# Kernel tuning notes

Measured on AMD Instinct MI355X. Metric: run time of the kernel, lower is better.

Reference implementation:

```python
import jax, jax.numpy as jnp
import numpy as np

E, NH, NL, NP = 256, 8, 4, 4
D = E // NH
SPATIAL_SHAPES = np.array([[100, 134], [50, 67], [25, 34], [13, 17]], dtype=np.int64)
B = 2


def setup_inputs() -> dict:
    key = jax.random.key(0)
    ks = jax.random.split(key, 12)
    Lin = int((SPATIAL_SHAPES[:, 0] * SPATIAL_SHAPES[:, 1]).sum())
    Lq = Lin
    s = 0.02
    return {
        'query': jax.random.normal(ks[0], (Lq, B, E), jnp.float32),
        'value': jax.random.normal(ks[1], (Lin, B, E), jnp.float32),
        'reference_points': jax.random.uniform(ks[2], (B, Lq, NL, 2), jnp.float32),
        'spatial_shapes': SPATIAL_SHAPES,
        'W_value': jax.random.normal(ks[3], (E, E), jnp.float32) * s,
        'b_value': jnp.zeros((E,), jnp.float32),
        'W_offset': jax.random.normal(ks[4], (E, NH * NL * NP * 2), jnp.float32) * s,
        'b_offset': jax.random.normal(ks[5], (NH * NL * NP * 2,), jnp.float32) * 0.5,
        'W_attn': jax.random.normal(ks[6], (E, NH * NL * NP), jnp.float32) * s,
        'b_attn': jnp.zeros((NH * NL * NP,), jnp.float32),
        'W_out': jax.random.normal(ks[7], (E, E), jnp.float32) * s,
        'b_out': jnp.zeros((E,), jnp.float32),
    }


def _ms_deform_attn(value, spatial_shapes, sampling_locations, attention_weights):
    # value: (B, Lin, NH, D); sampling_locations: (B, Lq, NH, NL, NP, 2) in [0,1]
    # attention_weights: (B, Lq, NH, NL, NP)
    b, _, nh, d = value.shape
    lq = sampling_locations.shape[1]
    npnt = sampling_locations.shape[4]
    shapes = np.asarray(spatial_shapes)
    out = jnp.zeros((b, nh, lq, d), value.dtype)
    start = 0
    for l in range(shapes.shape[0]):
        H, W = int(shapes[l, 0]), int(shapes[l, 1])
        vl = value[:, start:start + H * W].transpose(0, 2, 1, 3)  # (B, NH, H*W, D)
        loc = sampling_locations[:, :, :, l].transpose(0, 2, 1, 3, 4)  # (B, NH, Lq, P, 2)
        # grid_sample align_corners=False convention (matches CUDA kernel)
        x = loc[..., 0] * W - 0.5
        y = loc[..., 1] * H - 0.5
        x0 = jnp.floor(x)
        y0 = jnp.floor(y)
        dx = x - x0
        dy = y - y0
        x0i = x0.astype(jnp.int32)
        y0i = y0.astype(jnp.int32)
        acc = jnp.zeros((b, nh, lq, npnt, d), value.dtype)
        corners = [
            (x0i, y0i, (1.0 - dx) * (1.0 - dy)),
            (x0i + 1, y0i, dx * (1.0 - dy)),
            (x0i, y0i + 1, (1.0 - dx) * dy),
            (x0i + 1, y0i + 1, dx * dy),
        ]
        for xi, yi, w in corners:
            valid = ((xi >= 0) & (xi < W) & (yi >= 0) & (yi < H)).astype(value.dtype)
            idx = jnp.clip(yi, 0, W - 1 if False else H - 1) * 0  # placeholder removed below
            idx = jnp.clip(yi, 0, H - 1) * W + jnp.clip(xi, 0, W - 1)  # (B, NH, Lq, P)
            g = jnp.take_along_axis(vl, idx.reshape(b, nh, -1)[..., None], axis=2)
            g = g.reshape(b, nh, lq, npnt, d)
            acc = acc + g * (w * valid)[..., None]
        awl = attention_weights[:, :, :, l].transpose(0, 2, 1, 3)  # (B, NH, Lq, P)
        out = out + jnp.einsum('bhqpd,bhqp->bhqd', acc, awl)
        start += H * W
    return out.transpose(0, 2, 1, 3).reshape(b, lq, nh * d)  # (B, Lq, E)


def reference(query, value, reference_points, spatial_shapes,
              W_value, b_value, W_offset, b_offset, W_attn, b_attn, W_out, b_out):
    q = query.transpose(1, 0, 2)   # (B, Lq, E)
    v = value.transpose(1, 0, 2)   # (B, Lin, E)
    b, lq, _ = q.shape
    lin = v.shape[1]
    v = (v @ W_value + b_value).reshape(b, lin, NH, D)
    offsets = (q @ W_offset + b_offset).reshape(b, lq, NH, NL, NP, 2)
    attn = (q @ W_attn + b_attn).reshape(b, lq, NH, NL, NP)
    attn = jax.nn.softmax(attn, axis=-1)  # softmax over points (as in source)
    shapes_f = jnp.asarray(np.asarray(spatial_shapes), jnp.float32)
    offset_normalizer = jnp.stack([shapes_f[:, 1], shapes_f[:, 0]], -1)  # (NL, 2) = (w, h)
    loc = reference_points[:, :, None, :, None, :] + offsets / offset_normalizer[None, None, None, :, None, :]
    out = _ms_deform_attn(v, spatial_shapes, loc, attn)  # (B, Lq, E)
    out = out @ W_out + b_out
    return out.transpose(1, 0, 2)  # (Lq, B, E)
```

## Files before the change

### kernel.cpp

```cpp
#include <hip/hip_runtime.h>
#include <math.h>

#define LQ    17821
#define MROWS 35642
#define KD    256

typedef __attribute__((ext_vector_type(8))) short bf16x8;
typedef __attribute__((ext_vector_type(4))) float f32x4;

__device__ __forceinline__ short f2bf(float f) {
  union { float f; unsigned u; } c; c.f = f;
  unsigned u = c.u;
  return (short)((u + 0x7fffu + ((u >> 16) & 1u)) >> 16);
}
__device__ __forceinline__ float bf2f(short s) {
  union { unsigned u; float f; } c;
  c.u = ((unsigned)(unsigned short)s) << 16;
  return c.f;
}

__global__ __launch_bounds__(256) void wtrans_all(
    const float* __restrict__ Wv, const float* __restrict__ Woff,
    const float* __restrict__ Wat, const float* __restrict__ Wout,
    const float* __restrict__ boff, const float* __restrict__ bat,
    short* __restrict__ wT, float* __restrict__ fbias)
{
  int sel = blockIdx.y;
  int idx = blockIdx.x * 256 + threadIdx.x;
  if (sel == 4) {
    if (idx < 384) fbias[idx] = (idx < 256) ? boff[idx] : bat[idx - 256];
    return;
  }
  const float* W = sel == 0 ? Wv : sel == 1 ? Woff : sel == 2 ? Wat : Wout;
  short* Wt = wT + (sel == 0 ? 0 : sel == 1 ? 65536 : sel == 2 ? 131072 : 163840);
  int N = (sel == 2) ? 128 : 256;
  if (idx < N * 256) {
    int n = idx >> 8, k = idx & 255;
    Wt[idx] = f2bf(W[k * N + n]);
  }
}

template<bool A_F32>
__global__ __launch_bounds__(256, 2) void gemm_fullk(
    const void* __restrict__ A0, const void* __restrict__ A1,
    const short* __restrict__ Bt0, const short* __restrict__ Bt1,
    const float* __restrict__ bias0, const float* __restrict__ bias1,
    short* __restrict__ out0, float* __restrict__ out1,
    int M, int N1, int gybase)
{
  __shared__ bf16x8 As[32 * 128];

  const int tid = threadIdx.x;
  const int gy = blockIdx.y + gybase;
  const bool sel0 = gy < 2;
  const void* A = sel0 ? A0 : A1;
  const short* Bt = sel0 ? Bt0 : Bt1;
  const float* bias = sel0 ? bias0 : bias1;
  const int bn = (sel0 ? gy : gy - 2) * 128;
  const int bm = blockIdx.x * 128;

  {
    const int r = tid >> 1;
    const int h2 = tid & 1;
    const size_t arow = (size_t)min(bm + r, M - 1) * KD;
#pragma unroll
    for (int i = 0; i < 16; ++i) {
      const int s = h2 * 16 + i;
      bf16x8 v;
      if (A_F32) {
        const float* ap = (const float*)A + arow + s * 8;
        float4 p0 = *(const float4*)ap;
        float4 p1 = *(const float4*)(ap + 4);
        v[0] = f2bf(p0.x); v[1] = f2bf(p0.y); v[2] = f2bf(p0.z); v[3] = f2bf(p0.w);
        v[4] = f2bf(p1.x); v[5] = f2bf(p1.y); v[6] = f2bf(p1.z); v[7] = f2bf(p1.w);
      } else {
        v = *(const bf16x8*)((const short*)A + arow + s * 8);
      }
      As[s * 128 + (r ^ (s & 7))] = v;
    }
  }
  __syncthreads();

  const int lane = tid & 63;
  const int wave = tid >> 6;
  const int wm = (wave & 1) * 64;
  const int wn = (wave >> 1) * 64;
  const int ln = lane & 15;
  const int lq = lane >> 4;

  f32x4 acc[4][4];
#pragma unroll
  for (int i = 0; i < 4; ++i)
#pragma unroll
    for (int j = 0; j < 4; ++j) acc[i][j] = (f32x4){0.f, 0.f, 0.f, 0.f};

  bf16x8 af[2][4], bf[2][4];

#define LD_A(kk, dst)                                                        \
  {                                                                          \
    const int sA = (kk) * 4 + lq;                                            \
    const int swz = sA & 7;                                                  \
    _Pragma("unroll")                                                        \
    for (int i = 0; i < 4; ++i)                                              \
      dst[i] = As[sA * 128 + ((wm + i * 16 + ln) ^ swz)];                    \
  }
#define LD_B(kk, dst)                                                        \
  {                                                                          \
    _Pragma("unroll")                                                        \
    for (int j = 0; j < 4; ++j)                                              \
      dst[j] = *(const bf16x8*)(Bt + (size_t)(bn + wn + j * 16 + ln) * KD +  \
                                (kk) * 32 + lq * 8);                         \
  }

  LD_A(0, af[0]);
  LD_B(0, bf[0]);
#pragma unroll
  for (int kk = 0; kk < 8; ++kk) {
    const int cur = kk & 1, nxt = cur ^ 1;
    if (kk < 7) {
      LD_B(kk + 1, bf[nxt]);
      LD_A(kk + 1, af[nxt]);
    }
#pragma unroll
    for (int i = 0; i < 4; ++i)
#pragma unroll
      for (int j = 0; j < 4; ++j)
        acc[i][j] = __builtin_amdgcn_mfma_f32_16x16x32_bf16(af[cur][i], bf[cur][j], acc[i][j], 0, 0, 0);
  }
#undef LD_A
#undef LD_B

  const int N = sel0 ? 256 : N1;
#pragma unroll
  for (int j = 0; j < 4; ++j) {
    const int col = bn + wn + j * 16 + ln;
    const float bb = bias[col];
#pragma unroll
    for (int i = 0; i < 4; ++i) {
      const int row0 = bm + wm + i * 16 + lq * 4;
#pragma unroll
      for (int r = 0; r < 4; ++r) {
        const int row = row0 + r;
        if (row < M) {
          float v = acc[i][j][r] + bb;
          if (sel0)
            out0[(size_t)row * 256 + col] = f2bf(v);
          else
            out1[(size_t)row * N + col] = v;
        }
      }
    }
  }
}

__global__ __launch_bounds__(256) void msda_sample(
    const short* __restrict__ vproj, const float* __restrict__ oa,
    const float* __restrict__ refp, short* __restrict__ out)
{
  static constexpr int LVL_H[4] = {100, 50, 25, 13};
  static constexpr int LVL_W[4] = {134, 67, 34, 17};
  static constexpr int LVL_S[4] = {0, 13400, 16750, 17600};

  __shared__ int4   s_off[8 * 8 * 17];
  __shared__ float4 s_w[8 * 8 * 17];

  const int tid = threadIdx.x;
  const int m0 = blockIdx.x * 8;

#pragma unroll
  for (int it = 0; it < 4; ++it) {
    int w = tid + it * 256;
    int mr = w >> 7;
    int rest = w & 127;
    int h = rest >> 4;
    int lp = rest & 15;
    int l = lp >> 2;
    int p = lp & 3;
    int m = m0 + mr;
    if (m < MROWS) {
      int b = m & 1, q = m >> 1;
      const int Hl = LVL_H[l], Wl = LVL_W[l], Sl = LVL_S[l];
      const float fW = (float)Wl, fH = (float)Hl;

      float4 av = *(const float4*)(oa + (size_t)m * 384 + 256 + h * 16 + l * 4);
      float a0 = av.x, a1 = av.y, a2 = av.z, a3 = av.w;
      float mx = fmaxf(fmaxf(a0, a1), fmaxf(a2, a3));
      a0 = __expf(a0 - mx); a1 = __expf(a1 - mx);
      a2 = __expf(a2 - mx); a3 = __expf(a3 - mx);
      float sel = (p == 0) ? a0 : (p == 1) ? a1 : (p == 2) ? a2 : a3;
      float aw = sel / (a0 + a1 + a2 + a3);

      const float* oPtr = oa + (size_t)m * 384 + h * 32 + l * 8 + p * 2;
      float ox = oPtr[0], oy = oPtr[1];
      const float* rPtr = refp + ((size_t)b * LQ + q) * 8 + l * 2;
      float rx = rPtr[0], ry = rPtr[1];

      float x = (rx + ox / fW) * fW - 0.5f;
      float y = (ry + oy / fH) * fH - 0.5f;
      float x0f = floorf(x), y0f = floorf(y);
      float dx = x - x0f, dy = y - y0f;
      int x0 = (int)x0f, y0 = (int)y0f;
      int x1 = x0 + 1, y1 = y0 + 1;

      float w00 = (1.f - dx) * (1.f - dy) * aw;
      float w10 = dx * (1.f - dy) * aw;
      float w01 = (1.f - dx) * dy * aw;
      float w11 = dx * dy * aw;

      bool vx0 = (x0 >= 0) & (x0 < Wl);
      bool vx1 = (x1 >= 0) & (x1 < Wl);
      bool vy0 = (y0 >= 0) & (y0 < Hl);
      bool vy1 = (y1 >= 0) & (y1 < Hl);
      int cx0 = min(max(x0, 0), Wl - 1);
      int cx1 = min(max(x1, 0), Wl - 1);
      int cy0 = min(max(y0, 0), Hl - 1);
      int cy1 = min(max(y1, 0), Hl - 1);

      int r0 = Sl + cy0 * Wl;
      int r1 = Sl + cy1 * Wl;
      int e = (mr * 8 + h) * 17 + lp;
      s_off[e] = make_int4(((r0 + cx0) * 2 + b) << 8,
                           ((r0 + cx1) * 2 + b) << 8,
                           ((r1 + cx0) * 2 + b) << 8,
                           ((r1 + cx1) * 2 + b) << 8);
      s_w[e] = make_float4((vy0 & vx0) ? w00 : 0.f,
                           (vy0 & vx1) ? w10 : 0.f,
                           (vy1 & vx0) ? w01 : 0.f,
                           (vy1 & vx1) ? w11 : 0.f);
    }
  }
  __syncthreads();

  const int mr = tid >> 5;
  const int t = tid & 31;
  const int h = t >> 2;
  const int dq = t & 3;
  const int m = m0 + mr;
  if (m >= MROWS) return;

  const int laneOff = h * 32 + dq * 8;
  const int ebase = (mr * 8 + h) * 17;
  float acc[8];
#pragma unroll
  for (int e = 0; e < 8; ++e) acc[e] = 0.f;

#pragma unroll 4
  for (int lp = 0; lp < 16; ++lp) {
    int4 off = s_off[ebase + lp];
    float4 wv = s_w[ebase + lp];
    bf16x8 u00 = *(const bf16x8*)(vproj + off.x + laneOff);
    bf16x8 u10 = *(const bf16x8*)(vproj + off.y + laneOff);
    bf16x8 u01 = *(const bf16x8*)(vproj + off.z + laneOff);
    bf16x8 u11 = *(const bf16x8*)(vproj + off.w + laneOff);
#pragma unroll
    for (int e = 0; e < 8; ++e) {
      acc[e] = fmaf(wv.x, bf2f(u00[e]), acc[e]);
      acc[e] = fmaf(wv.y, bf2f(u10[e]), acc[e]);
      acc[e] = fmaf(wv.z, bf2f(u01[e]), acc[e]);
      acc[e] = fmaf(wv.w, bf2f(u11[e]), acc[e]);
    }
  }

  bf16x8 o;
#pragma unroll
  for (int e = 0; e < 8; ++e) o[e] = f2bf(acc[e]);
  *(bf16x8*)(out + (size_t)m * 256 + laneOff) = o;
}

extern "C" void kernel_launch(void* const* d_in, const int* in_sizes, int n_in,
                              void* d_out, int out_size, void* d_ws, size_t ws_size,
                              hipStream_t stream)
{
  const float* query = (const float*)d_in[0];
  const float* value = (const float*)d_in[1];
  const float* refp  = (const float*)d_in[2];
  const float* Wv   = (const float*)d_in[4];
  const float* bv   = (const float*)d_in[5];
  const float* Woff = (const float*)d_in[6];
  const float* boff = (const float*)d_in[7];
  const float* Wat  = (const float*)d_in[8];
  const float* bat  = (const float*)d_in[9];
  const float* Wout = (const float*)d_in[10];
  const float* bout = (const float*)d_in[11];
  float* out = (float*)d_out;

  const size_t NELT = (size_t)MROWS * 256;
  short* wT    = (short*)d_ws;
  float* fbias = (float*)(wT + 229376);
  short* vproj = (short*)(fbias + 384);
  short* accb  = vproj + NELT;
  float* oa    = (float*)(accb + NELT);

  dim3 blk(256, 1, 1);
  int gm = (MROWS + 127) / 128;

  wtrans_all<<<dim3(256, 5), blk, 0, stream>>>(Wv, Woff, Wat, Wout, boff, bat, wT, fbias);

  gemm_fullk<true><<<dim3(gm, 5), blk, 0, stream>>>(
      value, query, wT, wT + 65536, bv, fbias, vproj, oa, MROWS, 384, 0);

  msda_sample<<<dim3((MROWS + 7) / 8), blk, 0, stream>>>(vproj, oa, refp, accb);

  gemm_fullk<false><<<dim3(gm, 2), blk, 0, stream>>>(
      accb, accb, wT + 163840, wT + 163840, bout, bout, nullptr, out, MROWS, 256, 2);
}
```

Measured before the change: 330.8 us.

## Pre-convert activations to bf16 and stage GEMM tiles via direct global-to-LDS loads

```diff
diff --git a/kernel.cpp b/kernel.cpp
--- a/kernel.cpp
+++ b/kernel.cpp
@@ -7,6 +7,7 @@
 
 typedef __attribute__((ext_vector_type(8))) short bf16x8;
 typedef __attribute__((ext_vector_type(4))) float f32x4;
+typedef unsigned int u32;
 
 __device__ __forceinline__ short f2bf(float f) {
   union { float f; unsigned u; } c; c.f = f;
@@ -17,6 +18,27 @@
   union { unsigned u; float f; } c;
   c.u = ((unsigned)(unsigned short)s) << 16;
   return c.f;
+}
+
+__device__ __forceinline__ void gld_lds16(const short* g, short* l) {
+  __builtin_amdgcn_global_load_lds(
+      (const __attribute__((address_space(1))) u32*)g,
+      (__attribute__((address_space(3))) u32*)l, 16, 0, 0);
+}
+
+__global__ __launch_bounds__(256) void cvt_pair(
+    const float* __restrict__ q, const float* __restrict__ v,
+    short* __restrict__ qb, short* __restrict__ vb)
+{
+  const float* s = blockIdx.y ? v : q;
+  short* d = blockIdx.y ? vb : qb;
+  int i = (blockIdx.x * 256 + threadIdx.x) * 4;
+  if (i < MROWS * KD) {
+    float4 x = *(const float4*)(s + i);
+    short4 o;
+    o.x = f2bf(x.x); o.y = f2bf(x.y); o.z = f2bf(x.z); o.w = f2bf(x.w);
+    *(short4*)(d + i) = o;
+  }
 }
 
 __global__ __launch_bounds__(256) void wtrans_all(
@@ -40,51 +62,43 @@
   }
 }
 
-template<bool A_F32>
-__global__ __launch_bounds__(256, 2) void gemm_fullk(
-    const void* __restrict__ A0, const void* __restrict__ A1,
+__global__ __launch_bounds__(256, 3) void gemm_asy(
+    const short* __restrict__ A0, const short* __restrict__ A1,
     const short* __restrict__ Bt0, const short* __restrict__ Bt1,
     const float* __restrict__ bias0, const float* __restrict__ bias1,
     short* __restrict__ out0, float* __restrict__ out1,
-    int M, int N1, int gybase)
-{
-  __shared__ bf16x8 As[32 * 128];
+    int N1, int gybase)
+{
+  __shared__ short As[128 * 32];
+  __shared__ short Bs[128 * 32];
 
   const int tid = threadIdx.x;
   const int gy = blockIdx.y + gybase;
   const bool sel0 = gy < 2;
-  const void* A = sel0 ? A0 : A1;
+  const short* A = sel0 ? A0 : A1;
   const short* Bt = sel0 ? Bt0 : Bt1;
   const float* bias = sel0 ? bias0 : bias1;
   const int bn = (sel0 ? gy : gy - 2) * 128;
   const int bm = blockIdx.x * 128;
 
-  {
-    const int r = tid >> 1;
-    const int h2 = tid & 1;
-    const size_t arow = (size_t)min(bm + r, M - 1) * KD;
-#pragma unroll
-    for (int i = 0; i < 16; ++i) {
-      const int s = h2 * 16 + i;
-      bf16x8 v;
-      if (A_F32) {
-        const float* ap = (const float*)A + arow + s * 8;
-        float4 p0 = *(const float4*)ap;
-        float4 p1 = *(const float4*)(ap + 4);
-        v[0] = f2bf(p0.x); v[1] = f2bf(p0.y); v[2] = f2bf(p0.z); v[3] = f2bf(p0.w);
-        v[4] = f2bf(p1.x); v[5] = f2bf(p1.y); v[6] = f2bf(p1.z); v[7] = f2bf(p1.w);
-      } else {
-        v = *(const bf16x8*)((const short*)A + arow + s * 8);
-      }
-      As[s * 128 + (r ^ (s & 7))] = v;
-    }
-  }
-  __syncthreads();
-
+  const int wv = tid >> 6;
   const int lane = tid & 63;
-  const int wave = tid >> 6;
-  const int wm = (wave & 1) * 64;
-  const int wn = (wave >> 1) * 64;
+
+  const int srow = lane >> 2;
+  const int skel = (lane & 3) * 8;
+  const int rA0 = min(bm + wv * 32 + srow, MROWS - 1);
+  const int rA1 = min(bm + wv * 32 + 16 + srow, MROWS - 1);
+  const short* gA0 = A + (size_t)rA0 * KD + skel;
+  const short* gA1 = A + (size_t)rA1 * KD + skel;
+  const short* gB0 = Bt + (size_t)(bn + wv * 32 + srow) * KD + skel;
+  const short* gB1 = Bt + (size_t)(bn + wv * 32 + 16 + srow) * KD + skel;
+  short* lA0 = &As[(wv * 32) * 32];
+  short* lA1 = &As[(wv * 32 + 16) * 32];
+  short* lB0 = &Bs[(wv * 32) * 32];
+  short* lB1 = &Bs[(wv * 32 + 16) * 32];
+
+  const int wm = (wv & 1) * 64;
+  const int wn = (wv >> 1) * 64;
   const int ln = lane & 15;
   const int lq = lane >> 4;
 
@@ -94,41 +108,27 @@
 #pragma unroll
     for (int j = 0; j < 4; ++j) acc[i][j] = (f32x4){0.f, 0.f, 0.f, 0.f};
 
-  bf16x8 af[2][4], bf[2][4];
-
-#define LD_A(kk, dst)                                                        \
-  {                                                                          \
-    const int sA = (kk) * 4 + lq;                                            \
-    const int swz = sA & 7;                                                  \
-    _Pragma("unroll")                                                        \
-    for (int i = 0; i < 4; ++i)                                              \
-      dst[i] = As[sA * 128 + ((wm + i * 16 + ln) ^ swz)];                    \
-  }
-#define LD_B(kk, dst)                                                        \
-  {                                                                          \
-    _Pragma("unroll")                                                        \
-    for (int j = 0; j < 4; ++j)                                              \
-      dst[j] = *(const bf16x8*)(Bt + (size_t)(bn + wn + j * 16 + ln) * KD +  \
-                                (kk) * 32 + lq * 8);                         \
-  }
-
-  LD_A(0, af[0]);
-  LD_B(0, bf[0]);
-#pragma unroll
-  for (int kk = 0; kk < 8; ++kk) {
-    const int cur = kk & 1, nxt = cur ^ 1;
-    if (kk < 7) {
-      LD_B(kk + 1, bf[nxt]);
-      LD_A(kk + 1, af[nxt]);
-    }
+  for (int k0 = 0; k0 < KD; k0 += 32) {
+    __syncthreads();
+    gld_lds16(gA0 + k0, lA0);
+    gld_lds16(gA1 + k0, lA1);
+    gld_lds16(gB0 + k0, lB0);
+    gld_lds16(gB1 + k0, lB1);
+    __syncthreads();
+
+    bf16x8 af[4], bfm[4];
 #pragma unroll
     for (int i = 0; i < 4; ++i)
+      af[i] = *(const bf16x8*)&As[(wm + i * 16 + ln) * 32 + lq * 8];
+#pragma unroll
+    for (int j = 0; j < 4; ++j)
+      bfm[j] = *(const bf16x8*)&Bs[(wn + j * 16 + ln) * 32 + lq * 8];
+#pragma unroll
+    for (int i = 0; i < 4; ++i)
 #pragma unroll
       for (int j = 0; j < 4; ++j)
-        acc[i][j] = __builtin_amdgcn_mfma_f32_16x16x32_bf16(af[cur][i], bf[cur][j], acc[i][j], 0, 0, 0);
-  }
-#undef LD_A
-#undef LD_B
+        acc[i][j] = __builtin_amdgcn_mfma_f32_16x16x32_bf16(af[i], bfm[j], acc[i][j], 0, 0, 0);
+  }
 
   const int N = sel0 ? 256 : N1;
 #pragma unroll
@@ -141,7 +141,7 @@
 #pragma unroll
       for (int r = 0; r < 4; ++r) {
         const int row = row0 + r;
-        if (row < M) {
+        if (row < MROWS) {
           float v = acc[i][j][r] + bb;
           if (sel0)
             out0[(size_t)row * 256 + col] = f2bf(v);
@@ -287,20 +287,23 @@
   const size_t NELT = (size_t)MROWS * 256;
   short* wT    = (short*)d_ws;
   float* fbias = (float*)(wT + 229376);
-  short* vproj = (short*)(fbias + 384);
-  short* accb  = vproj + NELT;
-  float* oa    = (float*)(accb + NELT);
+  short* qb    = (short*)(fbias + 384);
+  short* vb    = qb + NELT;
+  short* vproj = vb + NELT;
+  float* oa    = (float*)(vproj + NELT);
+  short* accb  = vb;
 
   dim3 blk(256, 1, 1);
   int gm = (MROWS + 127) / 128;
 
+  cvt_pair<<<dim3(8911, 2), blk, 0, stream>>>(query, value, qb, vb);
   wtrans_all<<<dim3(256, 5), blk, 0, stream>>>(Wv, Woff, Wat, Wout, boff, bat, wT, fbias);
 
-  gemm_fullk<true><<<dim3(gm, 5), blk, 0, stream>>>(
-      value, query, wT, wT + 65536, bv, fbias, vproj, oa, MROWS, 384, 0);
+  gemm_asy<<<dim3(gm, 5), blk, 0, stream>>>(
+      vb, qb, wT, wT + 65536, bv, fbias, vproj, oa, 384, 0);
 
   msda_sample<<<dim3((MROWS + 7) / 8), blk, 0, stream>>>(vproj, oa, refp, accb);
 
-  gemm_fullk<false><<<dim3(gm, 2), blk, 0, stream>>>(
-      accb, accb, wT + 163840, wT + 163840, bout, bout, nullptr, out, MROWS, 256, 2);
-}
+  gemm_asy<<<dim3(gm, 2), blk, 0, stream>>>(
+      accb, accb, wT + 163840, wT + 163840, bout, bout, nullptr, out, 256, 2);
+}
```

Result: faster. 296.2 us (-10.5%).
